# Optimization experiments

Hardware: AMD Instinct MI355X
Metric: run time of the kernel (lower is better)

Reference implementation:

```python
import jax, jax.numpy as jnp
import numpy as np

M, N_GRID, DIM = 32, 32, 128
N_SAMPLES = 100000


def setup_inputs() -> dict:
    key = jax.random.key(0)
    k1, k2 = jax.random.split(key)
    x = jax.random.normal(k1, (N_SAMPLES, DIM), dtype=jnp.float32)
    som_weights = jax.random.normal(k2, (M, N_GRID, DIM), dtype=jnp.float32)
    return {"x": x, "som_weights": som_weights}


def reference(x, som_weights):
    # MiniSom.activation_response([v]) puts a 1 at the best-matching unit
    # (argmin Euclidean distance over the m*n prototype grid), then flattens.
    # Batched equivalent: [N, K] squared distances -> argmin -> one-hot.
    K = som_weights.shape[0] * som_weights.shape[1]
    w = som_weights.reshape(K, -1)                       # [K, dim]
    x_sq = jnp.sum(x * x, axis=1, keepdims=True)         # [N, 1]
    w_sq = jnp.sum(w * w, axis=1)                        # [K]
    # squared Euclidean distance; argmin identical to argmin of true distance
    d2 = x_sq + w_sq[None, :] - 2.0 * (x @ w.T)          # [N, K]
    bmu = jnp.argmin(d2, axis=1)                         # [N]
    return jax.nn.one_hot(bmu, K, dtype=jnp.float32)     # [N, K]
```

## Files before the change

### kernel.cpp

```cpp
#include <hip/hip_runtime.h>


typedef __attribute__((ext_vector_type(8))) short bf16x8;
typedef __attribute__((ext_vector_type(4))) float f32x4;

#define SOM_K 1024
#define SOM_D 128
#define SOM_N 100000
#define MARGIN 0.02f
#define FLAG_CAP 8192

#define WS_WSQ   64
#define WS_W3    8192
#define WS_FLAGS 532480
#define WS_REC   565248

static __device__ __forceinline__ unsigned short f2bf(float f) {
    unsigned u = __float_as_uint(f);
    return (unsigned short)((u + 0x7FFFu + ((u >> 16) & 1u)) >> 16);
}
static __device__ __forceinline__ float bf2f(unsigned short h) {
    return __uint_as_float(((unsigned)h) << 16);
}

__global__ __launch_bounds__(256) void som_prep(
    const float* __restrict__ w, unsigned short* __restrict__ w3,
    float* __restrict__ wsq)
{
    __shared__ float ws_[16][SOM_D];
    const int nt = blockIdx.x;
    const int tid = threadIdx.x;

    const float* src = w + (size_t)nt * 16 * SOM_D;
    #pragma unroll
    for (int r = 0; r < 8; ++r) {
        const int e = r * 256 + tid;
        ws_[e >> 7][e & 127] = src[e];
    }
    __syncthreads();

    unsigned short* dst = w3 + (size_t)nt * 4096;
    #pragma unroll
    for (int r = 0; r < 2; ++r) {
        const int G = r * 256 + tid;
        const int s = G >> 6;
        const int l = G & 63;
        const int c = l & 15, q = l >> 4;
        bf16x8 v;
        #pragma unroll
        for (int j = 0; j < 8; ++j) {
            const int kk = 32 * s + 8 * q + j;
            const int d = kk & 127;
            const float f = ws_[c][d];
            const unsigned short h = f2bf(f);
            v[j] = (short)((kk & 128) ? f2bf(f - bf2f(h)) : h);
        }
        *(bf16x8*)(dst + G * 8) = v;
    }

    if (tid < 16) {
        double s = 0.0;
        #pragma unroll 16
        for (int d = 0; d < SOM_D; ++d) {
            double v = (double)ws_[tid][d];
            s += v * v;
        }
        wsq[nt * 16 + tid] = (float)s;
    }
}

#define TILE_BODY(B_, NT_)                                                     \
    {                                                                          \
        const int n0 = (NT_) * 16;                                             \
        const float wq = wsq[n0 + c];                                          \
        f32x4 a0 = {0.f, 0.f, 0.f, 0.f}, a1 = {0.f, 0.f, 0.f, 0.f};            \
        _Pragma("unroll")                                                      \
        for (int s = 0; s < 4; ++s) {                             \
            a0 = __builtin_amdgcn_mfma_f32_16x16x32_bf16(ah[0][s], B_[s], a0, 0, 0, 0); \
            a1 = __builtin_amdgcn_mfma_f32_16x16x32_bf16(ah[1][s], B_[s], a1, 0, 0, 0); \
        }                                                                      \
        _Pragma("unroll")                                                      \
        for (int s = 0; s < 4; ++s) {                             \
            a0 = __builtin_amdgcn_mfma_f32_16x16x32_bf16(ah[0][s], B_[4 + s], a0, 0, 0, 0); \
            a1 = __builtin_amdgcn_mfma_f32_16x16x32_bf16(ah[1][s], B_[4 + s], a1, 0, 0, 0); \
        }                                                                      \
        _Pragma("unroll")                                                      \
        for (int s = 0; s < 4; ++s) {          \
            a0 = __builtin_amdgcn_mfma_f32_16x16x32_bf16(al[0][s], B_[s], a0, 0, 0, 0); \
            a1 = __builtin_amdgcn_mfma_f32_16x16x32_bf16(al[1][s], B_[s], a1, 0, 0, 0); \
        }                                                                      \
        _Pragma("unroll")                                                      \
        for (int r = 0; r < 4; ++r) {                                          \
            float s0 = wq - 2.f * a0[r];                                       \
            if (s0 < best[0][r]) { sec[0][r] = best[0][r]; best[0][r] = s0; bk[0][r] = n0 + c; } \
            else if (s0 < sec[0][r]) sec[0][r] = s0;                           \
            float s1 = wq - 2.f * a1[r];                                       \
            if (s1 < best[1][r]) { sec[1][r] = best[1][r]; best[1][r] = s1; bk[1][r] = n0 + c; } \
            else if (s1 < sec[1][r]) sec[1][r] = s1;                           \
        }                                                                      \
    }

__global__ __launch_bounds__(64, 2) void som_gemm(
    const float* __restrict__ x,
    const unsigned short* __restrict__ w3,
    const float* __restrict__ wsq,
    float4* __restrict__ rec)
{
    const int lane = threadIdx.x;
    const int c = lane & 15;
    const int q = lane >> 4;
    const int R0 = blockIdx.x * 32;

    bf16x8 ah[2][4], al[2][4];
    #pragma unroll
    for (int g = 0; g < 2; ++g) {
        const float* xp = x + (size_t)(R0 + 16 * g + c) * SOM_D + 8 * q;
        #pragma unroll
        for (int s = 0; s < 4; ++s) {
            float4 v0 = *(const float4*)(xp + 32 * s);
            float4 v1 = *(const float4*)(xp + 32 * s + 4);
            float xv[8] = {v0.x, v0.y, v0.z, v0.w, v1.x, v1.y, v1.z, v1.w};
            bf16x8 hh, ll;
            #pragma unroll
            for (int j = 0; j < 8; ++j) {
                unsigned short h = f2bf(xv[j]);
                hh[j] = (short)h;
                ll[j] = (short)f2bf(xv[j] - bf2f(h));
            }
            ah[g][s] = hh; al[g][s] = ll;
        }
    }

    float best[2][4], sec[2][4];
    int bk[2][4];
    #pragma unroll
    for (int g = 0; g < 2; ++g)
        #pragma unroll
        for (int r = 0; r < 4; ++r) { best[g][r] = 1e30f; sec[g][r] = 1e30f; bk[g][r] = 0; }

    const unsigned short* wbase = w3 + lane * 8;

    bf16x8 bA[8], bB[8];
    #pragma unroll
    for (int s = 0; s < 8; ++s) bA[s] = *(const bf16x8*)(wbase + 512 * s);

    #pragma unroll 1
    for (int ntp = 0; ntp < 32; ++ntp) {
        const int ntE = 2 * ntp;
        const int ntO = ntE + 1;
        {
            const unsigned short* wp = wbase + (size_t)ntO * 4096;
            #pragma unroll
            for (int s = 0; s < 8; ++s) bB[s] = *(const bf16x8*)(wp + 512 * s);
        }
        TILE_BODY(bA, ntE)
        {
            const int ntN = (ntp < 31) ? ntE + 2 : 0;
            const unsigned short* wp = wbase + (size_t)ntN * 4096;
            #pragma unroll
            for (int s = 0; s < 8; ++s) bA[s] = *(const bf16x8*)(wp + 512 * s);
        }
        TILE_BODY(bB, ntO)
    }

    #pragma unroll
    for (int g = 0; g < 2; ++g) {
        #pragma unroll
        for (int r = 0; r < 4; ++r) {
            float b0v = best[g][r], s0v = sec[g][r];
            int k0 = bk[g][r];
            #pragma unroll
            for (int m = 1; m < 16; m <<= 1) {
                float ob = __shfl_xor(b0v, m);
                float os = __shfl_xor(s0v, m);
                int   ok = __shfl_xor(k0, m);
                if (ob < b0v || (ob == b0v && ok < k0)) {
                    s0v = fminf(b0v, os); b0v = ob; k0 = ok;
                } else {
                    s0v = fminf(s0v, ob);
                }
            }
            best[g][r] = b0v; sec[g][r] = s0v; bk[g][r] = k0;
        }
    }

    if (c == 0) {
        #pragma unroll
        for (int g = 0; g < 2; ++g) {
            #pragma unroll
            for (int r = 0; r < 4; ++r) {
                const int row = R0 + g * 16 + 4 * q + r;
                float4 rv;
                rv.x = best[g][r];
                rv.y = sec[g][r];
                rv.z = __int_as_float(bk[g][r]);
                rv.w = 0.f;
                rec[row] = rv;
            }
        }
    }
}

__global__ __launch_bounds__(256) void som_write(
    const float4* __restrict__ rec,
    float* __restrict__ out,
    int* __restrict__ flag_count,
    int* __restrict__ flag_list)
{
    const int lane = threadIdx.x & 63;
    const int wv   = threadIdx.x >> 6;
    const int row  = blockIdx.x * 4 + wv;

    const float4 r = rec[row];
    const int b = __float_as_int(r.z);

    if (lane == 0 && (r.y - r.x < MARGIN)) {
        int i = atomicAdd(flag_count, 1);
        if (i < FLAG_CAP) flag_list[i] = row;
    }

    f32x4* op = (f32x4*)(out + (size_t)row * SOM_K);
    #pragma unroll
    for (int j = 0; j < 4; ++j) {
        const int e = j * 64 + lane;
        f32x4 v = {0.f, 0.f, 0.f, 0.f};
        if ((b >> 2) == e) v[b & 3] = 1.0f;
        __builtin_nontemporal_store(v, op + e);
    }
}

__global__ __launch_bounds__(1024) void som_pass2(
    const float* __restrict__ x,
    const float* __restrict__ w,
    float* __restrict__ out,
    const int* __restrict__ flag_count,
    const int* __restrict__ flag_list)
{
    __shared__ float xs[SOM_D];
    __shared__ double rbest[16];
    __shared__ int    rk[16];

    const int tid  = threadIdx.x;
    const int lane = tid & 63;
    const int wv   = tid >> 6;
    int cnt = *flag_count;
    if (cnt > FLAG_CAP) cnt = FLAG_CAP;

    for (int i = blockIdx.x; i < cnt; i += gridDim.x) {
        const int row = flag_list[i];
        __syncthreads();
        if (tid < SOM_D) xs[tid] = x[(size_t)row * SOM_D + tid];
        __syncthreads();

        const float* wk = w + (size_t)tid * SOM_D;
        double s0 = 0.0, s1 = 0.0;
        #pragma unroll
        for (int d = 0; d < SOM_D; d += 4) {
            float4 wv4 = *(const float4*)(wk + d);
            double w0 = (double)wv4.x, w1 = (double)wv4.y;
            double w2 = (double)wv4.z, w3 = (double)wv4.w;
            s0 += w0 * (w0 - 2.0 * (double)xs[d])     + w2 * (w2 - 2.0 * (double)xs[d + 2]);
            s1 += w1 * (w1 - 2.0 * (double)xs[d + 1]) + w3 * (w3 - 2.0 * (double)xs[d + 3]);
        }
        double sc = s0 + s1;
        int bk = tid;

        #pragma unroll
        for (int off = 32; off > 0; off >>= 1) {
            double os = __shfl_down(sc, off);
            int    ok = __shfl_down(bk, off);
            if (os < sc || (os == sc && ok < bk)) { sc = os; bk = ok; }
        }
        if (lane == 0) { rbest[wv] = sc; rk[wv] = bk; }
        __syncthreads();

        if (tid == 0) {
            double b = rbest[0]; int k0 = rk[0];
            #pragma unroll
            for (int v = 1; v < 16; ++v) {
                if (rbest[v] < b || (rbest[v] == b && rk[v] < k0)) { b = rbest[v]; k0 = rk[v]; }
            }
            rk[0] = k0;
        }
        __syncthreads();
        const int bmu = rk[0];

        out[(size_t)row * SOM_K + tid] = (tid == bmu) ? 1.0f : 0.0f;
    }
}

extern "C" void kernel_launch(void* const* d_in, const int* in_sizes, int n_in,
                              void* d_out, int out_size, void* d_ws, size_t ws_size,
                              hipStream_t stream) {
    const float* x = (const float*)d_in[0];
    const float* w = (const float*)d_in[1];
    float* out = (float*)d_out;

    char* ws = (char*)d_ws;
    int*            flag_count = (int*)ws;
    float*          wsq        = (float*)(ws + WS_WSQ);
    unsigned short* w3         = (unsigned short*)(ws + WS_W3);
    int*            flag_list  = (int*)(ws + WS_FLAGS);
    float4*         rec        = (float4*)(ws + WS_REC);

    (void)hipMemsetAsync(d_ws, 0, 64, stream);

    som_prep<<<64, 256, 0, stream>>>(w, w3, wsq);
    som_gemm<<<3125, 64, 0, stream>>>(x, w3, wsq, rec);
    som_write<<<25000, 256, 0, stream>>>(rec, out, flag_count, flag_list);
    som_pass2<<<256, 1024, 0, stream>>>(x, w, out, flag_count, flag_list);
}
```

Before: 640.6 us.

## Fuse one-hot write into GEMM, zero output via memset, use 48-row tiles

Removes the separate som_write kernel and its record buffer. The output is now zeroed with hipMemsetAsync, and the GEMM kernel scatters the single 1.0 per row and appends near-tie rows to the flag list itself. Each wave now handles 48 rows instead of 32, so every loaded weight tile feeds three MFMA accumulator groups. This raises register pressure and leaves a partial tail block (2084 blocks), which is handled by clamping reads and guarding writes.

After: 680.0 us. 1.06x slower.

```diff
diff --git a/kernel.cpp b/kernel.cpp
--- a/kernel.cpp
+++ b/kernel.cpp
@@ -13,7 +13,6 @@
 #define WS_WSQ   64
 #define WS_W3    8192
 #define WS_FLAGS 532480
-#define WS_REC   565248
 
 static __device__ __forceinline__ unsigned short f2bf(float f) {
     unsigned u = __float_as_uint(f);
@@ -73,21 +72,26 @@
     {                                                                          \
         const int n0 = (NT_) * 16;                                             \
         const float wq = wsq[n0 + c];                                          \
-        f32x4 a0 = {0.f, 0.f, 0.f, 0.f}, a1 = {0.f, 0.f, 0.f, 0.f};            \
+        f32x4 a0 = {0.f, 0.f, 0.f, 0.f};                                       \
+        f32x4 a1 = {0.f, 0.f, 0.f, 0.f};                                       \
+        f32x4 a2 = {0.f, 0.f, 0.f, 0.f};                                       \
         _Pragma("unroll")                                                      \
         for (int s = 0; s < 4; ++s) {                             \
             a0 = __builtin_amdgcn_mfma_f32_16x16x32_bf16(ah[0][s], B_[s], a0, 0, 0, 0); \
             a1 = __builtin_amdgcn_mfma_f32_16x16x32_bf16(ah[1][s], B_[s], a1, 0, 0, 0); \
+            a2 = __builtin_amdgcn_mfma_f32_16x16x32_bf16(ah[2][s], B_[s], a2, 0, 0, 0); \
         }                                                                      \
         _Pragma("unroll")                                                      \
         for (int s = 0; s < 4; ++s) {                             \
             a0 = __builtin_amdgcn_mfma_f32_16x16x32_bf16(ah[0][s], B_[4 + s], a0, 0, 0, 0); \
             a1 = __builtin_amdgcn_mfma_f32_16x16x32_bf16(ah[1][s], B_[4 + s], a1, 0, 0, 0); \
+            a2 = __builtin_amdgcn_mfma_f32_16x16x32_bf16(ah[2][s], B_[4 + s], a2, 0, 0, 0); \
         }                                                                      \
         _Pragma("unroll")                                                      \
         for (int s = 0; s < 4; ++s) {          \
             a0 = __builtin_amdgcn_mfma_f32_16x16x32_bf16(al[0][s], B_[s], a0, 0, 0, 0); \
             a1 = __builtin_amdgcn_mfma_f32_16x16x32_bf16(al[1][s], B_[s], a1, 0, 0, 0); \
+            a2 = __builtin_amdgcn_mfma_f32_16x16x32_bf16(al[2][s], B_[s], a2, 0, 0, 0); \
         }                                                                      \
         _Pragma("unroll")                                                      \
         for (int r = 0; r < 4; ++r) {                                          \
@@ -97,6 +101,9 @@
             float s1 = wq - 2.f * a1[r];                                       \
             if (s1 < best[1][r]) { sec[1][r] = best[1][r]; best[1][r] = s1; bk[1][r] = n0 + c; } \
             else if (s1 < sec[1][r]) sec[1][r] = s1;                           \
+            float s2 = wq - 2.f * a2[r];                                       \
+            if (s2 < best[2][r]) { sec[2][r] = best[2][r]; best[2][r] = s2; bk[2][r] = n0 + c; } \
+            else if (s2 < sec[2][r]) sec[2][r] = s2;                           \
         }                                                                      \
     }
 
@@ -104,17 +111,21 @@
     const float* __restrict__ x,
     const unsigned short* __restrict__ w3,
     const float* __restrict__ wsq,
-    float4* __restrict__ rec)
+    float* __restrict__ out,
+    int* __restrict__ flag_count,
+    int* __restrict__ flag_list)
 {
     const int lane = threadIdx.x;
     const int c = lane & 15;
     const int q = lane >> 4;
-    const int R0 = blockIdx.x * 32;
-
-    bf16x8 ah[2][4], al[2][4];
-    #pragma unroll
-    for (int g = 0; g < 2; ++g) {
-        const float* xp = x + (size_t)(R0 + 16 * g + c) * SOM_D + 8 * q;
+    const int R0 = blockIdx.x * 48;
+
+    bf16x8 ah[3][4], al[3][4];
+    #pragma unroll
+    for (int g = 0; g < 3; ++g) {
+        int rbase = R0 + 16 * g + c;
+        if (rbase > SOM_N - 1) rbase = SOM_N - 1;
+        const float* xp = x + (size_t)rbase * SOM_D + 8 * q;
         #pragma unroll
         for (int s = 0; s < 4; ++s) {
             float4 v0 = *(const float4*)(xp + 32 * s);
@@ -131,10 +142,10 @@
         }
     }
 
-    float best[2][4], sec[2][4];
-    int bk[2][4];
-    #pragma unroll
-    for (int g = 0; g < 2; ++g)
+    float best[3][4], sec[3][4];
+    int bk[3][4];
+    #pragma unroll
+    for (int g = 0; g < 3; ++g)
         #pragma unroll
         for (int r = 0; r < 4; ++r) { best[g][r] = 1e30f; sec[g][r] = 1e30f; bk[g][r] = 0; }
 
@@ -164,7 +175,7 @@
     }
 
     #pragma unroll
-    for (int g = 0; g < 2; ++g) {
+    for (int g = 0; g < 3; ++g) {
         #pragma unroll
         for (int r = 0; r < 4; ++r) {
             float b0v = best[g][r], s0v = sec[g][r];
@@ -186,46 +197,19 @@
 
     if (c == 0) {
         #pragma unroll
-        for (int g = 0; g < 2; ++g) {
+        for (int g = 0; g < 3; ++g) {
             #pragma unroll
             for (int r = 0; r < 4; ++r) {
                 const int row = R0 + g * 16 + 4 * q + r;
-                float4 rv;
-                rv.x = best[g][r];
-                rv.y = sec[g][r];
-                rv.z = __int_as_float(bk[g][r]);
-                rv.w = 0.f;
-                rec[row] = rv;
-            }
-        }
-    }
-}
-
-__global__ __launch_bounds__(256) void som_write(
-    const float4* __restrict__ rec,
-    float* __restrict__ out,
-    int* __restrict__ flag_count,
-    int* __restrict__ flag_list)
-{
-    const int lane = threadIdx.x & 63;
-    const int wv   = threadIdx.x >> 6;
-    const int row  = blockIdx.x * 4 + wv;
-
-    const float4 r = rec[row];
-    const int b = __float_as_int(r.z);
-
-    if (lane == 0 && (r.y - r.x < MARGIN)) {
-        int i = atomicAdd(flag_count, 1);
-        if (i < FLAG_CAP) flag_list[i] = row;
-    }
-
-    f32x4* op = (f32x4*)(out + (size_t)row * SOM_K);
-    #pragma unroll
-    for (int j = 0; j < 4; ++j) {
-        const int e = j * 64 + lane;
-        f32x4 v = {0.f, 0.f, 0.f, 0.f};
-        if ((b >> 2) == e) v[b & 3] = 1.0f;
-        __builtin_nontemporal_store(v, op + e);
+                if (row < SOM_N) {
+                    if (sec[g][r] - best[g][r] < MARGIN) {
+                        int i = atomicAdd(flag_count, 1);
+                        if (i < FLAG_CAP) flag_list[i] = row;
+                    }
+                    out[(size_t)row * SOM_K + bk[g][r]] = 1.0f;
+                }
+            }
+        }
     }
 }
 
@@ -301,12 +285,13 @@
     float*          wsq        = (float*)(ws + WS_WSQ);
     unsigned short* w3         = (unsigned short*)(ws + WS_W3);
     int*            flag_list  = (int*)(ws + WS_FLAGS);
-    float4*         rec        = (float4*)(ws + WS_REC);
 
     (void)hipMemsetAsync(d_ws, 0, 64, stream);
+    (void)hipMemsetAsync(d_out, 0,
+                         (size_t)SOM_N * SOM_K * sizeof(float),
+                         stream);
 
     som_prep<<<64, 256, 0, stream>>>(w, w3, wsq);
-    som_gemm<<<3125, 64, 0, stream>>>(x, w3, wsq, rec);
-    som_write<<<25000, 256, 0, stream>>>(rec, out, flag_count, flag_list);
+    som_gemm<<<2084, 64, 0, stream>>>(x, w3, wsq, out, flag_count, flag_list);
     som_pass2<<<256, 1024, 0, stream>>>(x, w, out, flag_count, flag_list);
 }
```
